# Kernel tuning notes

Measured on AMD Instinct MI355X. Metric: run time of the kernel, lower is better.

The kernel has to match this reference:

```python
import jax, jax.numpy as jnp
import numpy as np

NUM_EXPERTS = 16
HIDDEN = 2048
INTER = 768
TOP_K = 8
TOKENS = 2048
BLOCK = 16  # FP4 quantization block size along the contraction dim

_FP4_LEVELS = jnp.array([0.0, 0.5, 1.0, 1.5, 2.0, 3.0, 4.0, 6.0], dtype=jnp.float32)
_FP4_MIDS = jnp.array([0.25, 0.75, 1.25, 1.75, 2.5, 3.5, 5.0], dtype=jnp.float32)


def fp4_fake_quant(x):
    """Blockwise FP4 (e2m1) quantize-dequantize along the last dim.

    Emulates quantize_to_fp4 + dequant inside fp4_matmul: per-16 block scale
    = amax/6 (6 = max e2m1 magnitude), round-to-nearest on the e2m1 grid.
    """
    shp = x.shape
    xb = x.reshape(shp[:-1] + (shp[-1] // BLOCK, BLOCK))
    amax = jnp.max(jnp.abs(xb), axis=-1, keepdims=True)
    scale = jnp.where(amax > 0, amax / 6.0, 1.0)
    v = xb / scale
    idx = jnp.digitize(jnp.abs(v), _FP4_MIDS)  # 0..7 bucket on e2m1 grid
    q = _FP4_LEVELS[idx] * jnp.sign(v)
    return (q * scale).reshape(shp)


def setup_inputs() -> dict:
    key = jax.random.key(0)
    k1, k2, k3, k4, k5 = jax.random.split(key, 5)
    hidden_states = jax.random.normal(k1, (TOKENS, HIDDEN), dtype=jnp.float32)
    top_k_index = jax.random.randint(k2, (TOKENS, TOP_K), 0, NUM_EXPERTS)
    w = jax.random.uniform(k3, (TOKENS, TOP_K), dtype=jnp.float32) + 1e-3
    top_k_weights = w / jnp.sum(w, axis=-1, keepdims=True)
    gate_up_proj = jax.random.normal(k4, (NUM_EXPERTS, 2 * INTER, HIDDEN), dtype=jnp.float32) * 0.02
    down_proj = jax.random.normal(k5, (NUM_EXPERTS, HIDDEN, INTER), dtype=jnp.float32) * 0.02
    return {
        "hidden_states": hidden_states,
        "top_k_index": top_k_index,
        "top_k_weights": top_k_weights,
        "gate_up_proj": gate_up_proj,
        "down_proj": down_proj,
    }


def reference(hidden_states, top_k_index, top_k_weights, gate_up_proj, down_proj):
    # Combine weight per (token, expert): sums duplicate top-k hits, exactly
    # matching the torch loop's index_add_ over (top_k_pos, token_idx) pairs.
    one_hot = jax.nn.one_hot(top_k_index, NUM_EXPERTS, dtype=hidden_states.dtype)  # [T,k,E]
    w_te = jnp.einsum("tke,tk->te", one_hot, top_k_weights)  # [T,E]

    xq = fp4_fake_quant(hidden_states)                 # activation FP4 (per-row blocks)
    wgu_q = fp4_fake_quant(gate_up_proj)               # [E,2I,H] weight FP4
    wd_q = fp4_fake_quant(down_proj)                   # [E,H,I]

    h = jnp.einsum("th,eoh->eto", xq, wgu_q)           # [E,T,2I]
    gate, up = h[..., :INTER], h[..., INTER:]
    act = jax.nn.silu(gate) * up                       # [E,T,I]
    aq = fp4_fake_quant(act)
    y = jnp.einsum("eti,ehi->eth", aq, wd_q)           # [E,T,H]
    out = jnp.einsum("eth,te->th", y, w_te)            # scatter-combine
    return out
```

## Files before the change

### kernel.cpp

```cpp
#include <hip/hip_runtime.h>
#include <hip/hip_fp16.h>
#include <cstdint>

#define T_TOK 2048
#define H_DIM 2048
#define I_DIM 768
#define N_EXP 16
#define TOPK  8

typedef _Float16 half8  __attribute__((ext_vector_type(8)));
typedef _Float16 half4v __attribute__((ext_vector_type(4)));
typedef float    f32x4  __attribute__((ext_vector_type(4)));

#define GLDS16(g, l)                                                        \
  __builtin_amdgcn_global_load_lds(                                         \
      (const __attribute__((address_space(1))) unsigned int*)(g),           \
      (__attribute__((address_space(3))) unsigned int*)(l), 16, 0, 0)

__device__ __forceinline__ float fp4_q(float x, float scale) {
  float v = x / scale;
  float a = fabsf(v);
  float q;
  if      (a < 0.25f) q = 0.0f;
  else if (a < 0.75f) q = 0.5f;
  else if (a < 1.25f) q = 1.0f;
  else if (a < 1.75f) q = 1.5f;
  else if (a < 2.5f)  q = 2.0f;
  else if (a < 3.5f)  q = 3.0f;
  else if (a < 5.0f)  q = 4.0f;
  else                q = 6.0f;
  return copysignf(q, v) * scale;
}

__global__ void zero_kernel(float* __restrict__ out, int* __restrict__ counts) {
  int gid = blockIdx.x * 256 + threadIdx.x;
  ((f32x4*)out)[gid] = (f32x4){0.f, 0.f, 0.f, 0.f};
  if (gid < N_EXP) counts[gid] = 0;
}

__global__ void router_kernel(const int* __restrict__ idx, const float* __restrict__ wts,
                              float* __restrict__ w_te, int* __restrict__ counts,
                              int* __restrict__ list) {
  int t = blockIdx.x * 256 + threadIdx.x;
  if (t >= T_TOK) return;
  int   id[TOPK];
  float w[TOPK];
#pragma unroll
  for (int k = 0; k < TOPK; ++k) { id[k] = idx[t * TOPK + k]; w[k] = wts[t * TOPK + k]; }
#pragma unroll
  for (int e = 0; e < N_EXP; ++e) {
    float acc = 0.f;
#pragma unroll
    for (int k = 0; k < TOPK; ++k) acc += (id[k] == e) ? w[k] : 0.0f;
    w_te[t * N_EXP + e] = acc;
    if (acc != 0.0f) {
      int pos = atomicAdd(&counts[e], 1);
      list[e * T_TOK + pos] = t;
    }
  }
}

__global__ void quant_kernel(const float* __restrict__ src, _Float16* __restrict__ dh,
                             _Float16* __restrict__ dl, int n4) {
  int gid = blockIdx.x * 256 + threadIdx.x;
  if (gid >= n4) return;
  f32x4 x = ((const f32x4*)src)[gid];
  float am = fmaxf(fmaxf(fabsf(x[0]), fabsf(x[1])), fmaxf(fabsf(x[2]), fabsf(x[3])));
  am = fmaxf(am, __shfl_xor(am, 1, 64));
  am = fmaxf(am, __shfl_xor(am, 2, 64));
  float scale = am > 0.0f ? am / 6.0f : 1.0f;
  half4v hv, lv;
#pragma unroll
  for (int j = 0; j < 4; ++j) {
    float xq = fp4_q(x[j], scale);
    _Float16 h = (_Float16)xq;
    hv[j] = h;
    lv[j] = (_Float16)(xq - (float)h);
  }
  ((half4v*)dh)[gid] = hv;
  if (dl) ((half4v*)dl)[gid] = lv;
}

__launch_bounds__(256, 2)
__global__ void gemm1_kernel(const _Float16* __restrict__ xh, const _Float16* __restrict__ xl,
                             const _Float16* __restrict__ wh, const _Float16* __restrict__ wl,
                             const int* __restrict__ counts, const int* __restrict__ list,
                             _Float16* __restrict__ aq) {
  __shared__ __align__(16) _Float16 sAh[128 * 64];
  __shared__ __align__(16) _Float16 sAl[128 * 64];
  __shared__ __align__(16) _Float16 sBh[128 * 64];
  __shared__ __align__(16) _Float16 sBl[128 * 64];
  __shared__ int s_tok[128];

  const int e = blockIdx.z, tile = blockIdx.y;
  const int cnt = counts[e];
  const int row0 = tile * 128;
  if (row0 >= cnt) return;
  const int nvalid = min(128, cnt - row0);
  const int n0  = blockIdx.x * 64;
  const int tid = threadIdx.x;
  const int wave = tid >> 6, lane = tid & 63;

  if (tid < 128) {
    int r = (tid < nvalid) ? tid : 0;
    s_tok[tid] = list[e * T_TOK + row0 + r];
  }
  __syncthreads();

  size_t a_byte[4], b_byte[4];
  unsigned lds_off[4];
#pragma unroll
  for (int s = 0; s < 4; ++s) {
    int r = wave * 32 + s * 8 + (lane >> 3);
    int tok = s_tok[r];
    a_byte[s] = ((size_t)tok * H_DIM + (size_t)((lane & 7) * 8)) * 2;
    int grow = (r < 64) ? (e * 2 * I_DIM + n0 + r)
                        : (e * 2 * I_DIM + I_DIM + n0 + (r - 64));
    b_byte[s] = ((size_t)grow * H_DIM + (size_t)((lane & 7) * 8)) * 2;
    lds_off[s] = (unsigned)((wave * 32 + s * 8) * 64);
  }

  f32x4 accg[4][2] = {};
  f32x4 accu[4][2] = {};
  const int wm = wave >> 1, wn = wave & 1;

  unsigned a_off[4][2], bg_off[2][2], bu_off[2][2];
#pragma unroll
  for (int fr = 0; fr < 4; ++fr)
#pragma unroll
    for (int ks = 0; ks < 2; ++ks)
      a_off[fr][ks] = (wm * 64 + fr * 16 + (lane & 15)) * 64 + ks * 32 + (lane >> 4) * 8;
#pragma unroll
  for (int fn = 0; fn < 2; ++fn)
#pragma unroll
    for (int ks = 0; ks < 2; ++ks) {
      bg_off[fn][ks] = (wn * 32 + fn * 16 + (lane & 15)) * 64 + ks * 32 + (lane >> 4) * 8;
      bu_off[fn][ks] = bg_off[fn][ks] + 64 * 64;
    }

  for (int k0 = 0; k0 < H_DIM; k0 += 64) {
    __syncthreads();
    size_t kb = (size_t)k0 * 2;
#pragma unroll
    for (int s = 0; s < 4; ++s) {
      GLDS16((const char*)xh + a_byte[s] + kb, sAh + lds_off[s]);
      GLDS16((const char*)xl + a_byte[s] + kb, sAl + lds_off[s]);
      GLDS16((const char*)wh + b_byte[s] + kb, sBh + lds_off[s]);
      GLDS16((const char*)wl + b_byte[s] + kb, sBl + lds_off[s]);
    }
    __syncthreads();
#pragma unroll
    for (int ks = 0; ks < 2; ++ks) {
      half8 ah[4], al[4], bgh[2], bgl[2], buh[2], bul[2];
#pragma unroll
      for (int fr = 0; fr < 4; ++fr) {
        ah[fr] = *(const half8*)(sAh + a_off[fr][ks]);
        al[fr] = *(const half8*)(sAl + a_off[fr][ks]);
      }
#pragma unroll
      for (int fn = 0; fn < 2; ++fn) {
        bgh[fn] = *(const half8*)(sBh + bg_off[fn][ks]);
        bgl[fn] = *(const half8*)(sBl + bg_off[fn][ks]);
        buh[fn] = *(const half8*)(sBh + bu_off[fn][ks]);
        bul[fn] = *(const half8*)(sBl + bu_off[fn][ks]);
      }
#pragma unroll
      for (int fr = 0; fr < 4; ++fr)
#pragma unroll
        for (int fn = 0; fn < 2; ++fn) {
          accg[fr][fn] = __builtin_amdgcn_mfma_f32_16x16x32_f16(ah[fr], bgh[fn], accg[fr][fn], 0, 0, 0);
          accg[fr][fn] = __builtin_amdgcn_mfma_f32_16x16x32_f16(ah[fr], bgl[fn], accg[fr][fn], 0, 0, 0);
          accg[fr][fn] = __builtin_amdgcn_mfma_f32_16x16x32_f16(al[fr], bgh[fn], accg[fr][fn], 0, 0, 0);
          accu[fr][fn] = __builtin_amdgcn_mfma_f32_16x16x32_f16(ah[fr], buh[fn], accu[fr][fn], 0, 0, 0);
          accu[fr][fn] = __builtin_amdgcn_mfma_f32_16x16x32_f16(ah[fr], bul[fn], accu[fr][fn], 0, 0, 0);
          accu[fr][fn] = __builtin_amdgcn_mfma_f32_16x16x32_f16(al[fr], buh[fn], accu[fr][fn], 0, 0, 0);
        }
    }
  }

  __syncthreads();
  _Float16* sStage = sAh;
#pragma unroll
  for (int fr = 0; fr < 4; ++fr)
#pragma unroll
    for (int fn = 0; fn < 2; ++fn) {
      float act[4], am[4];
#pragma unroll
      for (int i = 0; i < 4; ++i) {
        float g = accg[fr][fn][i], u = accu[fr][fn][i];
        float sg = 1.0f / (1.0f + expf(-g));
        float si = g * sg;
        act[i] = si * u;
        am[i] = fabsf(act[i]);
      }
#pragma unroll
      for (int m = 1; m < 16; m <<= 1)
#pragma unroll
        for (int i = 0; i < 4; ++i) am[i] = fmaxf(am[i], __shfl_xor(am[i], m, 64));
      int col = wn * 32 + fn * 16 + (lane & 15);
#pragma unroll
      for (int i = 0; i < 4; ++i) {
        float scale = am[i] > 0.0f ? am[i] / 6.0f : 1.0f;
        float qv = fp4_q(act[i], scale);
        int row = wm * 64 + fr * 16 + (lane >> 4) * 4 + i;
        sStage[row * 64 + col] = (_Float16)qv;
      }
    }
  __syncthreads();
#pragma unroll
  for (int s = 0; s < 4; ++s) {
    int idx2 = tid + s * 256;
    int r = idx2 >> 3, c = idx2 & 7;
    if (r < nvalid) {
      *(uint4*)(aq + ((size_t)(e * T_TOK + row0 + r) * I_DIM + n0 + c * 8)) =
          *(const uint4*)(sStage + r * 64 + c * 8);
    }
  }
}

__launch_bounds__(256, 2)
__global__ void gemm2_kernel(const _Float16* __restrict__ aq, const _Float16* __restrict__ wdh,
                             const int* __restrict__ counts, const int* __restrict__ list,
                             const float* __restrict__ w_te, float* __restrict__ out) {
  __shared__ __align__(16) _Float16 sA[128 * 64];
  __shared__ __align__(16) _Float16 sB[128 * 64];
  __shared__ int   s_trow[128];
  __shared__ float s_wrow[128];

  const int e = blockIdx.z, tile = blockIdx.y;
  const int cnt = counts[e];
  const int row0 = tile * 128;
  if (row0 >= cnt) return;
  const int nvalid = min(128, cnt - row0);
  const int n1  = blockIdx.x * 128;
  const int tid = threadIdx.x;
  const int wave = tid >> 6, lane = tid & 63;

  if (tid < 128) {
    int r = (tid < nvalid) ? tid : 0;
    int t = list[e * T_TOK + row0 + r];
    s_trow[tid] = t;
    s_wrow[tid] = w_te[t * N_EXP + e];
  }

  size_t a_byte[4], b_byte[4];
  unsigned lds_off[4];
#pragma unroll
  for (int s = 0; s < 4; ++s) {
    int r = wave * 32 + s * 8 + (lane >> 3);
    int ra = (r < nvalid) ? r : 0;
    a_byte[s] = (((size_t)(e * T_TOK + row0 + ra)) * I_DIM + (size_t)((lane & 7) * 8)) * 2;
    b_byte[s] = (((size_t)(e * H_DIM + n1 + r)) * I_DIM + (size_t)((lane & 7) * 8)) * 2;
    lds_off[s] = (unsigned)((wave * 32 + s * 8) * 64);
  }

  f32x4 acc[4][4] = {};
  const int wm = wave >> 1, wn = wave & 1;
  unsigned a_off[4][2], b_off[4][2];
#pragma unroll
  for (int fr = 0; fr < 4; ++fr)
#pragma unroll
    for (int ks = 0; ks < 2; ++ks)
      a_off[fr][ks] = (wm * 64 + fr * 16 + (lane & 15)) * 64 + ks * 32 + (lane >> 4) * 8;
#pragma unroll
  for (int fn = 0; fn < 4; ++fn)
#pragma unroll
    for (int ks = 0; ks < 2; ++ks)
      b_off[fn][ks] = (wn * 64 + fn * 16 + (lane & 15)) * 64 + ks * 32 + (lane >> 4) * 8;

  for (int k0 = 0; k0 < I_DIM; k0 += 64) {
    __syncthreads();
    size_t kb = (size_t)k0 * 2;
#pragma unroll
    for (int s = 0; s < 4; ++s) {
      GLDS16((const char*)aq  + a_byte[s] + kb, sA + lds_off[s]);
      GLDS16((const char*)wdh + b_byte[s] + kb, sB + lds_off[s]);
    }
    __syncthreads();
#pragma unroll
    for (int ks = 0; ks < 2; ++ks) {
      half8 a[4], b[4];
#pragma unroll
      for (int fr = 0; fr < 4; ++fr) a[fr] = *(const half8*)(sA + a_off[fr][ks]);
#pragma unroll
      for (int fn = 0; fn < 4; ++fn) b[fn] = *(const half8*)(sB + b_off[fn][ks]);
#pragma unroll
      for (int fr = 0; fr < 4; ++fr)
#pragma unroll
        for (int fn = 0; fn < 4; ++fn)
          acc[fr][fn] = __builtin_amdgcn_mfma_f32_16x16x32_f16(a[fr], b[fn], acc[fr][fn], 0, 0, 0);
    }
  }

#pragma unroll
  for (int fr = 0; fr < 4; ++fr) {
    int rb = wm * 64 + fr * 16 + (lane >> 4) * 4;
#pragma unroll
    for (int i = 0; i < 4; ++i) {
      int row = rb + i;
      if (row < nvalid) {
        int t = s_trow[row];
        float w = s_wrow[row];
#pragma unroll
        for (int fn = 0; fn < 4; ++fn) {
          int col = n1 + wn * 64 + fn * 16 + (lane & 15);
          unsafeAtomicAdd(&out[(size_t)t * H_DIM + col], w * acc[fr][fn][i]);
        }
      }
    }
  }
}

extern "C" void kernel_launch(void* const* d_in, const int* in_sizes, int n_in,
                              void* d_out, int out_size, void* d_ws, size_t ws_size,
                              hipStream_t stream) {
  const float* hs  = (const float*)d_in[0];
  const int*   tki = (const int*)d_in[1];
  const float* tkw = (const float*)d_in[2];
  const float* wgu = (const float*)d_in[3];
  const float* wd  = (const float*)d_in[4];
  float* out = (float*)d_out;

  char* ws = (char*)d_ws;
  size_t off = 0;
  auto alloc = [&](size_t bytes) -> void* {
    void* p = ws + off;
    off += bytes;
    off = (off + 255) & ~(size_t)255;
    return p;
  };
  int*      counts = (int*)alloc(N_EXP * 4);
  float*    w_te   = (float*)alloc((size_t)T_TOK * N_EXP * 4);
  int*      list   = (int*)alloc((size_t)N_EXP * T_TOK * 4);
  _Float16* xh     = (_Float16*)alloc((size_t)T_TOK * H_DIM * 2);
  _Float16* xl     = (_Float16*)alloc((size_t)T_TOK * H_DIM * 2);
  _Float16* wguh   = (_Float16*)alloc((size_t)N_EXP * 2 * I_DIM * H_DIM * 2);
  _Float16* wgul   = (_Float16*)alloc((size_t)N_EXP * 2 * I_DIM * H_DIM * 2);
  _Float16* wdh    = (_Float16*)alloc((size_t)N_EXP * H_DIM * I_DIM * 2);
  _Float16* aqb    = (_Float16*)alloc((size_t)N_EXP * T_TOK * I_DIM * 2);
  if (off > ws_size) return;

  zero_kernel<<<dim3(4096), dim3(256), 0, stream>>>(out, counts);
  router_kernel<<<dim3(8), dim3(256), 0, stream>>>(tki, tkw, w_te, counts, list);
  quant_kernel<<<dim3(4096), dim3(256), 0, stream>>>(hs, xh, xl, T_TOK * H_DIM / 4);
  quant_kernel<<<dim3(49152), dim3(256), 0, stream>>>(wgu, wguh, wgul, N_EXP * 2 * I_DIM * H_DIM / 4);
  quant_kernel<<<dim3(24576), dim3(256), 0, stream>>>(wd, wdh, (_Float16*)nullptr, N_EXP * H_DIM * I_DIM / 4);
  gemm1_kernel<<<dim3(I_DIM / 64, 16, N_EXP), dim3(256), 0, stream>>>(xh, xl, wguh, wgul, counts, list, aqb);
  gemm2_kernel<<<dim3(H_DIM / 128, 16, N_EXP), dim3(256), 0, stream>>>(aqb, wdh, counts, list, w_te, out);
}
```

Baseline: 839.9 us.

## Double-buffer LDS with XOR swizzle and remap block grid in both MoE GEMMs

Both expert GEMMs now load K in 32-wide stages into two LDS buffers, prefetching the next stage while MFMAs run on the current one, with one barrier per stage instead of two. The LDS layout uses an XOR swizzle on 16-byte chunks to cut bank conflicts on fragment reads. The 3D grid is flattened to 1D and remapped so neighbouring blocks spread across XCDs and share weight tiles, and gemm2 asks for three blocks per CU via launch bounds. The cost is more barriers per unit of K from the smaller stages, and possible register pressure from the higher occupancy target.

```diff
diff --git a/kernel.cpp b/kernel.cpp
--- a/kernel.cpp
+++ b/kernel.cpp
@@ -32,6 +32,8 @@
   return copysignf(q, v) * scale;
 }
 
+__device__ __forceinline__ int swz_m(int r) { return (r & 3) ^ ((r >> 2) & 1); }
+
 __global__ void zero_kernel(float* __restrict__ out, int* __restrict__ counts) {
   int gid = blockIdx.x * 256 + threadIdx.x;
   ((f32x4*)out)[gid] = (f32x4){0.f, 0.f, 0.f, 0.f};
@@ -86,18 +88,20 @@
                              const _Float16* __restrict__ wh, const _Float16* __restrict__ wl,
                              const int* __restrict__ counts, const int* __restrict__ list,
                              _Float16* __restrict__ aq) {
-  __shared__ __align__(16) _Float16 sAh[128 * 64];
-  __shared__ __align__(16) _Float16 sAl[128 * 64];
-  __shared__ __align__(16) _Float16 sBh[128 * 64];
-  __shared__ __align__(16) _Float16 sBl[128 * 64];
+  __shared__ __align__(16) _Float16 smem[2][4][128 * 32];
   __shared__ int s_tok[128];
 
-  const int e = blockIdx.z, tile = blockIdx.y;
-  const int cnt = counts[e];
+  const int orig = blockIdx.x;
+  const int swz  = (orig & 7) * (3072 / 8) + (orig >> 3);
+  const int tile = swz & 15;
+  const int n0i  = (swz >> 4) % 12;
+  const int e    = swz / 192;
+
+  const int cnt  = counts[e];
   const int row0 = tile * 128;
   if (row0 >= cnt) return;
   const int nvalid = min(128, cnt - row0);
-  const int n0  = blockIdx.x * 64;
+  const int n0  = n0i * 64;
   const int tid = threadIdx.x;
   const int wave = tid >> 6, lane = tid & 63;
 
@@ -107,79 +111,90 @@
   }
   __syncthreads();
 
-  size_t a_byte[4], b_byte[4];
-  unsigned lds_off[4];
-#pragma unroll
-  for (int s = 0; s < 4; ++s) {
-    int r = wave * 32 + s * 8 + (lane >> 3);
+  size_t aG[2], bG[2];
+  unsigned ldsOff[2];
+#pragma unroll
+  for (int p = 0; p < 2; ++p) {
+    int q = tid + p * 256;
+    int r = q >> 2, c = q & 3;
+    int sc = c ^ swz_m(r);
+    ldsOff[p] = (unsigned)q * 8;
     int tok = s_tok[r];
-    a_byte[s] = ((size_t)tok * H_DIM + (size_t)((lane & 7) * 8)) * 2;
+    aG[p] = ((size_t)tok * H_DIM) * 2 + (size_t)(sc * 16);
     int grow = (r < 64) ? (e * 2 * I_DIM + n0 + r)
                         : (e * 2 * I_DIM + I_DIM + n0 + (r - 64));
-    b_byte[s] = ((size_t)grow * H_DIM + (size_t)((lane & 7) * 8)) * 2;
-    lds_off[s] = (unsigned)((wave * 32 + s * 8) * 64);
+    bG[p] = ((size_t)grow * H_DIM) * 2 + (size_t)(sc * 16);
+  }
+
+  const int wm = wave >> 1, wn = wave & 1;
+  const int kc = lane >> 4;
+  unsigned aRd[4], bgRd[2], buRd[2];
+#pragma unroll
+  for (int fr = 0; fr < 4; ++fr) {
+    int R = wm * 64 + fr * 16 + (lane & 15);
+    aRd[fr] = (unsigned)(R * 32 + (kc ^ swz_m(R)) * 8);
+  }
+#pragma unroll
+  for (int fn = 0; fn < 2; ++fn) {
+    int R = wn * 32 + fn * 16 + (lane & 15);
+    bgRd[fn] = (unsigned)(R * 32 + (kc ^ swz_m(R)) * 8);
+    int R2 = R + 64;
+    buRd[fn] = (unsigned)(R2 * 32 + (kc ^ swz_m(R2)) * 8);
   }
 
   f32x4 accg[4][2] = {};
   f32x4 accu[4][2] = {};
-  const int wm = wave >> 1, wn = wave & 1;
-
-  unsigned a_off[4][2], bg_off[2][2], bu_off[2][2];
-#pragma unroll
-  for (int fr = 0; fr < 4; ++fr)
-#pragma unroll
-    for (int ks = 0; ks < 2; ++ks)
-      a_off[fr][ks] = (wm * 64 + fr * 16 + (lane & 15)) * 64 + ks * 32 + (lane >> 4) * 8;
-#pragma unroll
-  for (int fn = 0; fn < 2; ++fn)
-#pragma unroll
-    for (int ks = 0; ks < 2; ++ks) {
-      bg_off[fn][ks] = (wn * 32 + fn * 16 + (lane & 15)) * 64 + ks * 32 + (lane >> 4) * 8;
-      bu_off[fn][ks] = bg_off[fn][ks] + 64 * 64;
-    }
-
-  for (int k0 = 0; k0 < H_DIM; k0 += 64) {
+
+#define STAGE1(buf, k0)                                                       \
+  do {                                                                        \
+    size_t kb = (size_t)(k0) * 2;                                             \
+    _Pragma("unroll") for (int p = 0; p < 2; ++p) {                           \
+      GLDS16((const char*)xh + aG[p] + kb, &smem[buf][0][0] + ldsOff[p]);     \
+      GLDS16((const char*)xl + aG[p] + kb, &smem[buf][1][0] + ldsOff[p]);     \
+      GLDS16((const char*)wh + bG[p] + kb, &smem[buf][2][0] + ldsOff[p]);     \
+      GLDS16((const char*)wl + bG[p] + kb, &smem[buf][3][0] + ldsOff[p]);     \
+    }                                                                         \
+  } while (0)
+
+  STAGE1(0, 0);
+  __syncthreads();
+  const int NT = H_DIM / 32;
+  for (int t = 0; t < NT; ++t) {
+    const int cur = t & 1;
+    if (t + 1 < NT) STAGE1(cur ^ 1, (t + 1) * 32);
+    const _Float16* sAh = &smem[cur][0][0];
+    const _Float16* sAl = &smem[cur][1][0];
+    const _Float16* sBh = &smem[cur][2][0];
+    const _Float16* sBl = &smem[cur][3][0];
+    half8 ah[4], al[4], bgh[2], bgl[2], buh[2], bul[2];
+#pragma unroll
+    for (int fr = 0; fr < 4; ++fr) {
+      ah[fr] = *(const half8*)(sAh + aRd[fr]);
+      al[fr] = *(const half8*)(sAl + aRd[fr]);
+    }
+#pragma unroll
+    for (int fn = 0; fn < 2; ++fn) {
+      bgh[fn] = *(const half8*)(sBh + bgRd[fn]);
+      bgl[fn] = *(const half8*)(sBl + bgRd[fn]);
+      buh[fn] = *(const half8*)(sBh + buRd[fn]);
+      bul[fn] = *(const half8*)(sBl + buRd[fn]);
+    }
+#pragma unroll
+    for (int fr = 0; fr < 4; ++fr)
+#pragma unroll
+      for (int fn = 0; fn < 2; ++fn) {
+        accg[fr][fn] = __builtin_amdgcn_mfma_f32_16x16x32_f16(ah[fr], bgh[fn], accg[fr][fn], 0, 0, 0);
+        accg[fr][fn] = __builtin_amdgcn_mfma_f32_16x16x32_f16(ah[fr], bgl[fn], accg[fr][fn], 0, 0, 0);
+        accg[fr][fn] = __builtin_amdgcn_mfma_f32_16x16x32_f16(al[fr], bgh[fn], accg[fr][fn], 0, 0, 0);
+        accu[fr][fn] = __builtin_amdgcn_mfma_f32_16x16x32_f16(ah[fr], buh[fn], accu[fr][fn], 0, 0, 0);
+        accu[fr][fn] = __builtin_amdgcn_mfma_f32_16x16x32_f16(ah[fr], bul[fn], accu[fr][fn], 0, 0, 0);
+        accu[fr][fn] = __builtin_amdgcn_mfma_f32_16x16x32_f16(al[fr], buh[fn], accu[fr][fn], 0, 0, 0);
+      }
     __syncthreads();
-    size_t kb = (size_t)k0 * 2;
-#pragma unroll
-    for (int s = 0; s < 4; ++s) {
-      GLDS16((const char*)xh + a_byte[s] + kb, sAh + lds_off[s]);
-      GLDS16((const char*)xl + a_byte[s] + kb, sAl + lds_off[s]);
-      GLDS16((const char*)wh + b_byte[s] + kb, sBh + lds_off[s]);
-      GLDS16((const char*)wl + b_byte[s] + kb, sBl + lds_off[s]);
-    }
-    __syncthreads();
-#pragma unroll
-    for (int ks = 0; ks < 2; ++ks) {
-      half8 ah[4], al[4], bgh[2], bgl[2], buh[2], bul[2];
-#pragma unroll
-      for (int fr = 0; fr < 4; ++fr) {
-        ah[fr] = *(const half8*)(sAh + a_off[fr][ks]);
-        al[fr] = *(const half8*)(sAl + a_off[fr][ks]);
-      }
-#pragma unroll
-      for (int fn = 0; fn < 2; ++fn) {
-        bgh[fn] = *(const half8*)(sBh + bg_off[fn][ks]);
-        bgl[fn] = *(const half8*)(sBl + bg_off[fn][ks]);
-        buh[fn] = *(const half8*)(sBh + bu_off[fn][ks]);
-        bul[fn] = *(const half8*)(sBl + bu_off[fn][ks]);
-      }
-#pragma unroll
-      for (int fr = 0; fr < 4; ++fr)
-#pragma unroll
-        for (int fn = 0; fn < 2; ++fn) {
-          accg[fr][fn] = __builtin_amdgcn_mfma_f32_16x16x32_f16(ah[fr], bgh[fn], accg[fr][fn], 0, 0, 0);
-          accg[fr][fn] = __builtin_amdgcn_mfma_f32_16x16x32_f16(ah[fr], bgl[fn], accg[fr][fn], 0, 0, 0);
-          accg[fr][fn] = __builtin_amdgcn_mfma_f32_16x16x32_f16(al[fr], bgh[fn], accg[fr][fn], 0, 0, 0);
-          accu[fr][fn] = __builtin_amdgcn_mfma_f32_16x16x32_f16(ah[fr], buh[fn], accu[fr][fn], 0, 0, 0);
-          accu[fr][fn] = __builtin_amdgcn_mfma_f32_16x16x32_f16(ah[fr], bul[fn], accu[fr][fn], 0, 0, 0);
-          accu[fr][fn] = __builtin_amdgcn_mfma_f32_16x16x32_f16(al[fr], buh[fn], accu[fr][fn], 0, 0, 0);
-        }
-    }
-  }
-
-  __syncthreads();
-  _Float16* sStage = sAh;
+  }
+#undef STAGE1
+
+  _Float16* sStage = &smem[0][0][0];
 #pragma unroll
   for (int fr = 0; fr < 4; ++fr)
 #pragma unroll
@@ -189,8 +204,7 @@
       for (int i = 0; i < 4; ++i) {
         float g = accg[fr][fn][i], u = accu[fr][fn][i];
         float sg = 1.0f / (1.0f + expf(-g));
-        float si = g * sg;
-        act[i] = si * u;
+        act[i] = g * sg * u;
         am[i] = fabsf(act[i]);
       }
 #pragma unroll
@@ -218,21 +232,25 @@
   }
 }
 
-__launch_bounds__(256, 2)
+__launch_bounds__(256, 3)
 __global__ void gemm2_kernel(const _Float16* __restrict__ aq, const _Float16* __restrict__ wdh,
                              const int* __restrict__ counts, const int* __restrict__ list,
                              const float* __restrict__ w_te, float* __restrict__ out) {
-  __shared__ __align__(16) _Float16 sA[128 * 64];
-  __shared__ __align__(16) _Float16 sB[128 * 64];
+  __shared__ __align__(16) _Float16 smem[2][2][128 * 32];
   __shared__ int   s_trow[128];
   __shared__ float s_wrow[128];
 
-  const int e = blockIdx.z, tile = blockIdx.y;
-  const int cnt = counts[e];
+  const int orig = blockIdx.x;
+  const int swz  = (orig & 7) * (4096 / 8) + (orig >> 3);
+  const int tile = swz & 15;
+  const int n1i  = (swz >> 4) & 15;
+  const int e    = swz >> 8;
+
+  const int cnt  = counts[e];
   const int row0 = tile * 128;
   if (row0 >= cnt) return;
   const int nvalid = min(128, cnt - row0);
-  const int n1  = blockIdx.x * 128;
+  const int n1  = n1i * 128;
   const int tid = threadIdx.x;
   const int wave = tid >> 6, lane = tid & 63;
 
@@ -243,54 +261,65 @@
     s_wrow[tid] = w_te[t * N_EXP + e];
   }
 
-  size_t a_byte[4], b_byte[4];
-  unsigned lds_off[4];
-#pragma unroll
-  for (int s = 0; s < 4; ++s) {
-    int r = wave * 32 + s * 8 + (lane >> 3);
+  size_t aG[2], bG[2];
+  unsigned ldsOff[2];
+#pragma unroll
+  for (int p = 0; p < 2; ++p) {
+    int q = tid + p * 256;
+    int r = q >> 2, c = q & 3;
+    int sc = c ^ swz_m(r);
+    ldsOff[p] = (unsigned)q * 8;
     int ra = (r < nvalid) ? r : 0;
-    a_byte[s] = (((size_t)(e * T_TOK + row0 + ra)) * I_DIM + (size_t)((lane & 7) * 8)) * 2;
-    b_byte[s] = (((size_t)(e * H_DIM + n1 + r)) * I_DIM + (size_t)((lane & 7) * 8)) * 2;
-    lds_off[s] = (unsigned)((wave * 32 + s * 8) * 64);
+    aG[p] = ((size_t)(e * T_TOK + row0 + ra) * I_DIM) * 2 + (size_t)(sc * 16);
+    bG[p] = ((size_t)(e * H_DIM + n1 + r) * I_DIM) * 2 + (size_t)(sc * 16);
+  }
+
+  const int wm = wave >> 1, wn = wave & 1;
+  const int kc = lane >> 4;
+  unsigned aRd[4], bRd[4];
+#pragma unroll
+  for (int fr = 0; fr < 4; ++fr) {
+    int R = wm * 64 + fr * 16 + (lane & 15);
+    aRd[fr] = (unsigned)(R * 32 + (kc ^ swz_m(R)) * 8);
+  }
+#pragma unroll
+  for (int fn = 0; fn < 4; ++fn) {
+    int R = wn * 64 + fn * 16 + (lane & 15);
+    bRd[fn] = (unsigned)(R * 32 + (kc ^ swz_m(R)) * 8);
   }
 
   f32x4 acc[4][4] = {};
-  const int wm = wave >> 1, wn = wave & 1;
-  unsigned a_off[4][2], b_off[4][2];
-#pragma unroll
-  for (int fr = 0; fr < 4; ++fr)
-#pragma unroll
-    for (int ks = 0; ks < 2; ++ks)
-      a_off[fr][ks] = (wm * 64 + fr * 16 + (lane & 15)) * 64 + ks * 32 + (lane >> 4) * 8;
-#pragma unroll
-  for (int fn = 0; fn < 4; ++fn)
-#pragma unroll
-    for (int ks = 0; ks < 2; ++ks)
-      b_off[fn][ks] = (wn * 64 + fn * 16 + (lane & 15)) * 64 + ks * 32 + (lane >> 4) * 8;
-
-  for (int k0 = 0; k0 < I_DIM; k0 += 64) {
+
+#define STAGE2(buf, k0)                                                       \
+  do {                                                                        \
+    size_t kb = (size_t)(k0) * 2;                                             \
+    _Pragma("unroll") for (int p = 0; p < 2; ++p) {                           \
+      GLDS16((const char*)aq  + aG[p] + kb, &smem[buf][0][0] + ldsOff[p]);    \
+      GLDS16((const char*)wdh + bG[p] + kb, &smem[buf][1][0] + ldsOff[p]);    \
+    }                                                                         \
+  } while (0)
+
+  STAGE2(0, 0);
+  __syncthreads();
+  const int NT = I_DIM / 32;
+  for (int t = 0; t < NT; ++t) {
+    const int cur = t & 1;
+    if (t + 1 < NT) STAGE2(cur ^ 1, (t + 1) * 32);
+    const _Float16* sA = &smem[cur][0][0];
+    const _Float16* sB = &smem[cur][1][0];
+    half8 a[4], b[4];
+#pragma unroll
+    for (int fr = 0; fr < 4; ++fr) a[fr] = *(const half8*)(sA + aRd[fr]);
+#pragma unroll
+    for (int fn = 0; fn < 4; ++fn) b[fn] = *(const half8*)(sB + bRd[fn]);
+#pragma unroll
+    for (int fr = 0; fr < 4; ++fr)
+#pragma unroll
+      for (int fn = 0; fn < 4; ++fn)
+        acc[fr][fn] = __builtin_amdgcn_mfma_f32_16x16x32_f16(a[fr], b[fn], acc[fr][fn], 0, 0, 0);
     __syncthreads();
-    size_t kb = (size_t)k0 * 2;
-#pragma unroll
-    for (int s = 0; s < 4; ++s) {
-      GLDS16((const char*)aq  + a_byte[s] + kb, sA + lds_off[s]);
-      GLDS16((const char*)wdh + b_byte[s] + kb, sB + lds_off[s]);
-    }
-    __syncthreads();
-#pragma unroll
-    for (int ks = 0; ks < 2; ++ks) {
-      half8 a[4], b[4];
-#pragma unroll
-      for (int fr = 0; fr < 4; ++fr) a[fr] = *(const half8*)(sA + a_off[fr][ks]);
-#pragma unroll
-      for (int fn = 0; fn < 4; ++fn) b[fn] = *(const half8*)(sB + b_off[fn][ks]);
-#pragma unroll
-      for (int fr = 0; fr < 4; ++fr)
-#pragma unroll
-        for (int fn = 0; fn < 4; ++fn)
-          acc[fr][fn] = __builtin_amdgcn_mfma_f32_16x16x32_f16(a[fr], b[fn], acc[fr][fn], 0, 0, 0);
-    }
-  }
+  }
+#undef STAGE2
 
 #pragma unroll
   for (int fr = 0; fr < 4; ++fr) {
@@ -345,6 +374,6 @@
   quant_kernel<<<dim3(4096), dim3(256), 0, stream>>>(hs, xh, xl, T_TOK * H_DIM / 4);
   quant_kernel<<<dim3(49152), dim3(256), 0, stream>>>(wgu, wguh, wgul, N_EXP * 2 * I_DIM * H_DIM / 4);
   quant_kernel<<<dim3(24576), dim3(256), 0, stream>>>(wd, wdh, (_Float16*)nullptr, N_EXP * H_DIM * I_DIM / 4);
-  gemm1_kernel<<<dim3(I_DIM / 64, 16, N_EXP), dim3(256), 0, stream>>>(xh, xl, wguh, wgul, counts, list, aqb);
-  gemm2_kernel<<<dim3(H_DIM / 128, 16, N_EXP), dim3(256), 0, stream>>>(aqb, wdh, counts, list, w_te, out);
-}
+  gemm1_kernel<<<dim3(3072), dim3(256), 0, stream>>>(xh, xl, wguh, wgul, counts, list, aqb);
+  gemm2_kernel<<<dim3(4096), dim3(256), 0, stream>>>(aqb, wdh, counts, list, w_te, out);
+}
```

Result: faster. 822.9 us (-2.0%).
